# Performance work log

Hardware: AMD Instinct MI355X
Metric: run time of the kernel (lower is better)

## Reference

```python
import jax, jax.numpy as jnp
import numpy as np

B, S, HID = 2, 4096, 2048
NH, NKV, HD = 32, 8, 64
GROUPS = NH // NKV
ROPE_THETA = 10000.0


def _rope_cos_sin(seq_len, dim, dtype):
    inv_freq = 1.0 / (ROPE_THETA ** (jnp.arange(0, dim, 2, dtype=jnp.float32) / dim))
    pos = jnp.arange(seq_len, dtype=jnp.float32)
    freqs = pos[:, None] * inv_freq[None, :]          # [S, D/2]
    emb = jnp.concatenate([freqs, freqs], axis=-1)    # [S, D]
    return jnp.cos(emb).astype(dtype), jnp.sin(emb).astype(dtype)


def _rotate_half(x):
    x1, x2 = jnp.split(x, 2, axis=-1)
    return jnp.concatenate([-x2, x1], axis=-1)


def _apply_rope(x, cos, sin):
    # x: [B, H, S, D]; cos/sin: [S, D]
    return x * cos[None, None] + _rotate_half(x) * sin[None, None]


def kappa(x):
    return jax.nn.elu(x) + 1.0


def setup_inputs() -> dict:
    key = jax.random.key(0)
    ks = jax.random.split(key, 6)
    sc = 0.02
    return {
        "hidden_states": jax.random.normal(ks[0], (B, S, HID), jnp.float32),
        "Wq": jax.random.normal(ks[1], (HID, NH * HD), jnp.float32) * sc,
        "Wk": jax.random.normal(ks[2], (HID, NKV * HD), jnp.float32) * sc,
        "Wv": jax.random.normal(ks[3], (HID, NKV * HD), jnp.float32) * sc,
        "Wphi": jax.random.normal(ks[4], (HID, HID), jnp.float32) * sc,
        "Wo": jax.random.normal(ks[5], (HID, HID), jnp.float32) * sc,
    }


def reference(hidden_states, Wq, Wk, Wv, Wphi, Wo):
    bsz, q_len, _ = hidden_states.shape

    q = (hidden_states @ Wq).reshape(bsz, q_len, NH, HD).transpose(0, 2, 1, 3)   # [B,NH,S,D]
    k = (hidden_states @ Wk).reshape(bsz, q_len, NKV, HD).transpose(0, 2, 1, 3)  # [B,NKV,S,D]
    v = (hidden_states @ Wv).reshape(bsz, q_len, NKV, HD).transpose(0, 2, 1, 3)

    cos, sin = _rope_cos_sin(q_len, HD, hidden_states.dtype)
    q = _apply_rope(q, cos, sin)
    k = _apply_rope(k, cos, sin)

    # repeat_kv for GQA: [B,NKV,S,D] -> [B,NH,S,D]
    k = jnp.repeat(k, GROUPS, axis=1)
    v = jnp.repeat(v, GROUPS, axis=1)

    Qk = kappa(q)   # [B,NH,S,D]
    Kk = kappa(k)

    Qg = Qk.mean(axis=2)                                # [B,NH,D] global query
    logits = jnp.einsum("bnd,bnsd->bns", Qg, Kk)        # [B,NH,S]
    alpha = jax.nn.softmax(logits, axis=-1) * float(q_len)

    # KV aggregation: [B,NH,D,D] state
    outer_sum = jnp.einsum("bns,bnsd,bnsf->bndf", alpha, Kk, v)
    result_attn = jnp.einsum("bnsd,bndf->bnsf", Qk, outer_sum)  # [B,NH,S,D]

    X_phi = (hidden_states @ Wphi).reshape(bsz, q_len, NH, HD).transpose(0, 2, 1, 3)
    ctx = (X_phi * result_attn).transpose(0, 2, 1, 3).reshape(bsz, q_len, HID)
    return ctx @ Wo
```

## Files before the change

### kernel.cpp

```cpp
#include <hip/hip_runtime.h>
#include <hip/hip_bf16.h>

#define B_ 2
#define S_ 4096
#define HID_ 2048
#define NH_ 32
#define NKV_ 8
#define HD_ 64
#define GROUPS_ 4
#define NCH_ 32

typedef short short8 __attribute__((ext_vector_type(8)));
typedef float floatx4 __attribute__((ext_vector_type(4)));

__device__ __forceinline__ float bf2f(unsigned short u){
  union { unsigned int i; float f; } v; v.i = ((unsigned int)u) << 16; return v.f;
}
__device__ __forceinline__ unsigned short f2bf(float f){
  union { float f; unsigned int i; } v; v.f = f;
  unsigned int i = v.i;
  unsigned int r = (i + 0x7fffu + ((i >> 16) & 1u)) >> 16;
  return (unsigned short)r;
}

__device__ __forceinline__ void async_copy16(unsigned short* lds, const unsigned short* g){
  __builtin_amdgcn_global_load_lds((const __attribute__((address_space(1))) void*)g,
                                   (__attribute__((address_space(3))) void*)lds,
                                   16, 0, 0);
}

__global__ void conv_bf16(const float* __restrict__ x, unsigned short* __restrict__ y, int n4){
  int i = blockIdx.x * 256 + threadIdx.x;
  if (i < n4){
    float4 v = ((const float4*)x)[i];
    ushort4 o;
    o.x = f2bf(v.x); o.y = f2bf(v.y); o.z = f2bf(v.z); o.w = f2bf(v.w);
    ((ushort4*)y)[i] = o;
  }
}

__global__ void transpose_to_bf16(const float* __restrict__ W, unsigned short* __restrict__ Wt,
                                  int K, int N){
  __shared__ float tile[32][33];
  int n0 = blockIdx.x * 32, k0 = blockIdx.y * 32;
  int tx = threadIdx.x, ty = threadIdx.y;
  #pragma unroll
  for (int j = 0; j < 4; j++)
    tile[ty + j*8][tx] = W[(size_t)(k0 + ty + j*8) * N + n0 + tx];
  __syncthreads();
  #pragma unroll
  for (int j = 0; j < 4; j++)
    Wt[(size_t)(n0 + ty + j*8) * K + k0 + tx] = f2bf(tile[tx][ty + j*8]);
}

#define GTILE 16384

__global__ __launch_bounds__(512, 2) void gemm256(
    const unsigned short* __restrict__ A, const unsigned short* __restrict__ Bt,
    void* __restrict__ Cv, int M, int N, int K, int cbf16)
{
  __shared__ __align__(16) unsigned short As[2 * GTILE];
  __shared__ __align__(16) unsigned short Bs[2 * GTILE];

  const int tid = threadIdx.x;
  const int w = tid >> 6, lane = tid & 63;
  const int wr = w >> 2, wc = w & 3;
  const int l15 = lane & 15, quad = lane >> 4;

  const int nbx = N >> 8;
  int flat = blockIdx.y * nbx + blockIdx.x;
  int nwg  = nbx * (M >> 8);
  int cpx  = nwg >> 3;
  int swz  = (flat & 7) * cpx + (flat >> 3);
  int bx = swz % nbx, by = swz / nbx;
  const int m0 = by << 8, n0 = bx << 8;

  const int srow = (w << 3) + (lane >> 3);
  const int scc  = (lane & 7) ^ (lane >> 3);
  const unsigned short* gA = A  + (size_t)(m0 + srow) * K + scc * 8;
  const unsigned short* gB = Bt + (size_t)(n0 + srow) * K + scc * 8;
  const size_t rs64  = (size_t)64  * K;
  const size_t rs128 = (size_t)128 * K;
  unsigned short* lA0 = As + (w << 9);
  unsigned short* lB0 = Bs + (w << 9);

#define STAGE_A(bsel, h, t) do { \
    unsigned short* _d = lA0 + (bsel) * GTILE + (h) * 8192; \
    const unsigned short* _g = gA + (size_t)(h) * rs128 + (size_t)(t) * 64; \
    async_copy16(_d, _g); \
    async_copy16(_d + 4096, _g + rs64); \
  } while (0)
#define STAGE_B(bsel, h, t) do { \
    unsigned short* _d = lB0 + (bsel) * GTILE + (h) * 8192; \
    const unsigned short* _g = gB + (size_t)(h) * rs128 + (size_t)(t) * 64; \
    async_copy16(_d, _g); \
    async_copy16(_d + 4096, _g + rs64); \
  } while (0)
#define SCHED0 __builtin_amdgcn_sched_barrier(0)

  const int ks0  = ((quad     ^ (lane & 7)) << 3);
  const int ks1  = (((4+quad) ^ (lane & 7)) << 3);
  const int arow = (wr * 128 + l15) * 64;
  const int brow = (wc * 64  + l15) * 64;

  floatx4 acc[8][4] = {};
  short8 af[8][2], bfr[4][2];

  const int nt = K >> 6;

  STAGE_A(0, 0, 0); STAGE_A(0, 1, 0); STAGE_B(0, 0, 0); STAGE_B(0, 1, 0);
  if (nt > 1){
    STAGE_A(1, 0, 1); STAGE_A(1, 1, 1); STAGE_B(1, 0, 1); STAGE_B(1, 1, 1);
    asm volatile("s_waitcnt vmcnt(8)" ::: "memory");
  } else {
    asm volatile("s_waitcnt vmcnt(0)" ::: "memory");
  }
  SCHED0;
  __builtin_amdgcn_s_barrier();
  SCHED0;

  for (int T = 0; T < nt; ++T){
    const int cb = T & 1;
    const unsigned short* Ab = As + cb * GTILE;
    const unsigned short* Bb = Bs + cb * GTILE;

    #pragma unroll
    for (int m = 0; m < 4; ++m){
      af[m][0] = *(const short8*)(Ab + arow + m * 1024 + ks0);
      af[m][1] = *(const short8*)(Ab + arow + m * 1024 + ks1);
    }
    #pragma unroll
    for (int n = 0; n < 2; ++n){
      bfr[n][0] = *(const short8*)(Bb + brow + n * 1024 + ks0);
      bfr[n][1] = *(const short8*)(Bb + brow + n * 1024 + ks1);
    }
    SCHED0; __builtin_amdgcn_s_barrier(); SCHED0;
    __builtin_amdgcn_s_setprio(1);
    #pragma unroll
    for (int m = 0; m < 4; ++m)
      #pragma unroll
      for (int n = 0; n < 2; ++n){
        acc[m][n] = __builtin_amdgcn_mfma_f32_16x16x32_bf16(af[m][0], bfr[n][0], acc[m][n], 0, 0, 0);
        acc[m][n] = __builtin_amdgcn_mfma_f32_16x16x32_bf16(af[m][1], bfr[n][1], acc[m][n], 0, 0, 0);
      }
    __builtin_amdgcn_s_setprio(0);
    SCHED0; __builtin_amdgcn_s_barrier(); SCHED0;

    #pragma unroll
    for (int m = 0; m < 4; ++m){
      af[4+m][0] = *(const short8*)(Ab + arow + (4+m) * 1024 + ks0);
      af[4+m][1] = *(const short8*)(Ab + arow + (4+m) * 1024 + ks1);
    }
    #pragma unroll
    for (int n = 0; n < 2; ++n){
      bfr[2+n][0] = *(const short8*)(Bb + brow + (2+n) * 1024 + ks0);
      bfr[2+n][1] = *(const short8*)(Bb + brow + (2+n) * 1024 + ks1);
    }
    SCHED0; __builtin_amdgcn_s_barrier(); SCHED0;
    __builtin_amdgcn_s_setprio(1);
    #pragma unroll
    for (int m = 0; m < 4; ++m)
      #pragma unroll
      for (int n = 0; n < 2; ++n){
        acc[m][2+n] = __builtin_amdgcn_mfma_f32_16x16x32_bf16(af[m][0], bfr[2+n][0], acc[m][2+n], 0, 0, 0);
        acc[m][2+n] = __builtin_amdgcn_mfma_f32_16x16x32_bf16(af[m][1], bfr[2+n][1], acc[m][2+n], 0, 0, 0);
      }
    __builtin_amdgcn_s_setprio(0);
    SCHED0; __builtin_amdgcn_s_barrier(); SCHED0;

    if (T + 2 < nt){ STAGE_A(cb, 0, T + 2); STAGE_A(cb, 1, T + 2); }
    SCHED0; __builtin_amdgcn_s_barrier(); SCHED0;
    __builtin_amdgcn_s_setprio(1);
    #pragma unroll
    for (int m = 0; m < 4; ++m)
      #pragma unroll
      for (int n = 0; n < 2; ++n){
        acc[4+m][n] = __builtin_amdgcn_mfma_f32_16x16x32_bf16(af[4+m][0], bfr[n][0], acc[4+m][n], 0, 0, 0);
        acc[4+m][n] = __builtin_amdgcn_mfma_f32_16x16x32_bf16(af[4+m][1], bfr[n][1], acc[4+m][n], 0, 0, 0);
      }
    __builtin_amdgcn_s_setprio(0);
    SCHED0; __builtin_amdgcn_s_barrier(); SCHED0;

    if (T + 2 < nt){
      STAGE_B(cb, 0, T + 2); STAGE_B(cb, 1, T + 2);
      asm volatile("s_waitcnt vmcnt(8)" ::: "memory");
    } else {
      asm volatile("s_waitcnt vmcnt(0)" ::: "memory");
    }
    SCHED0; __builtin_amdgcn_s_barrier(); SCHED0;
    __builtin_amdgcn_s_setprio(1);
    #pragma unroll
    for (int m = 0; m < 4; ++m)
      #pragma unroll
      for (int n = 0; n < 2; ++n){
        acc[4+m][2+n] = __builtin_amdgcn_mfma_f32_16x16x32_bf16(af[4+m][0], bfr[2+n][0], acc[4+m][2+n], 0, 0, 0);
        acc[4+m][2+n] = __builtin_amdgcn_mfma_f32_16x16x32_bf16(af[4+m][1], bfr[2+n][1], acc[4+m][2+n], 0, 0, 0);
      }
    __builtin_amdgcn_s_setprio(0);
    SCHED0; __builtin_amdgcn_s_barrier(); SCHED0;
  }

#undef STAGE_A
#undef STAGE_B
#undef SCHED0

  if (cbf16){
    unsigned short* Cb = (unsigned short*)Cv;
    #pragma unroll
    for (int mi = 0; mi < 8; ++mi){
      const int row = m0 + wr * 128 + mi * 16 + quad * 4;
      #pragma unroll
      for (int ni = 0; ni < 4; ++ni){
        const int col = n0 + wc * 64 + ni * 16 + l15;
        #pragma unroll
        for (int r = 0; r < 4; ++r)
          Cb[(size_t)(row + r) * N + col] = f2bf(acc[mi][ni][r]);
      }
    }
  } else {
    float* Cf = (float*)Cv;
    #pragma unroll
    for (int mi = 0; mi < 8; ++mi){
      const int row = m0 + wr * 128 + mi * 16 + quad * 4;
      #pragma unroll
      for (int ni = 0; ni < 4; ++ni){
        const int col = n0 + wc * 64 + ni * 16 + l15;
        #pragma unroll
        for (int r = 0; r < 4; ++r)
          Cf[(size_t)(row + r) * N + col] = acc[mi][ni][r];
      }
    }
  }
}

__global__ void rope_kappa_q(const unsigned short* __restrict__ Qlin, unsigned short* __restrict__ Qk){
  int idx = blockIdx.x * 256 + threadIdx.x;
  int i = idx & 31;
  int n = (idx >> 5) & (NH_ - 1);
  int s = (idx >> 10) & (S_ - 1);
  int b = idx >> 22;
  float invf = exp2f(-(float)i * (13.287712379549449f / 32.0f));
  float ang = (float)s * invf;
  float c = cosf(ang), sn = sinf(ang);
  size_t in_o = ((size_t)(b * S_ + s) * NH_ + n) * HD_;
  float x1 = bf2f(Qlin[in_o + i]);
  float x2 = bf2f(Qlin[in_o + i + 32]);
  float r1 = x1 * c - x2 * sn;
  float r2 = x2 * c + x1 * sn;
  r1 = r1 > 0.f ? r1 + 1.f : __expf(r1);
  r2 = r2 > 0.f ? r2 + 1.f : __expf(r2);
  size_t o = ((size_t)(b * NH_ + n) * S_ + s) * HD_;
  Qk[o + i] = f2bf(r1);
  Qk[o + i + 32] = f2bf(r2);
}

__global__ void rope_kappa_k(const unsigned short* __restrict__ KVlin, unsigned short* __restrict__ Kk){
  int idx = blockIdx.x * 256 + threadIdx.x;
  int i = idx & 31;
  int kv = (idx >> 5) & (NKV_ - 1);
  int s = (idx >> 8) & (S_ - 1);
  int b = idx >> 20;
  float invf = exp2f(-(float)i * (13.287712379549449f / 32.0f));
  float ang = (float)s * invf;
  float c = cosf(ang), sn = sinf(ang);
  size_t in_o = (size_t)(b * S_ + s) * 1024 + kv * HD_;
  float x1 = bf2f(KVlin[in_o + i]);
  float x2 = bf2f(KVlin[in_o + i + 32]);
  float r1 = x1 * c - x2 * sn;
  float r2 = x2 * c + x1 * sn;
  r1 = r1 > 0.f ? r1 + 1.f : __expf(r1);
  r2 = r2 > 0.f ? r2 + 1.f : __expf(r2);
  size_t o = ((size_t)(b * NKV_ + kv) * S_ + s) * HD_;
  Kk[o + i] = f2bf(r1);
  Kk[o + i + 32] = f2bf(r2);
}

__global__ __launch_bounds__(256) void qg_mean(const unsigned short* __restrict__ Qk,
                                               float* __restrict__ Qg){
  int bn = blockIdx.x, chunk = blockIdx.y;
  int tid = threadIdx.x;
  int dgrp = tid & 7, sgrp = tid >> 3;
  const unsigned short* base = Qk + (size_t)bn * S_ * HD_
                             + (size_t)(chunk * 256 + sgrp) * HD_ + dgrp * 8;
  float acc[8] = {};
  #pragma unroll
  for (int i = 0; i < 8; i++){
    short8 v = *(const short8*)(base + (size_t)i * 32 * HD_);
    #pragma unroll
    for (int e = 0; e < 8; e++) acc[e] += bf2f((unsigned short)v[e]);
  }
  __shared__ float red[256][8];
  #pragma unroll
  for (int e = 0; e < 8; e++) red[tid][e] = acc[e];
  __syncthreads();
  if (tid < 64){
    int dg = tid >> 3, e = tid & 7;
    float s = 0.f;
    #pragma unroll
    for (int g = 0; g < 32; g++) s += red[g * 8 + dg][e];
    atomicAdd(&Qg[bn * 64 + tid], s * (1.0f / (float)S_));
  }
}

__global__ __launch_bounds__(256) void logits_kernel(const unsigned short* __restrict__ Kk,
                                                     const float* __restrict__ Qg,
                                                     float* __restrict__ logits){
  int bn = blockIdx.x, chunk = blockIdx.y;
  int b = bn / NH_, n = bn % NH_, kv = n / GROUPS_;
  int tid = threadIdx.x;
  __shared__ float qg[64];
  if (tid < 64) qg[tid] = Qg[bn * 64 + tid];
  __syncthreads();
  int s = chunk * 256 + tid;
  const unsigned short* row = Kk + ((size_t)(b * NKV_ + kv) * S_ + s) * HD_;
  float acc = 0.f;
  #pragma unroll
  for (int c = 0; c < 8; c++){
    short8 v = *(const short8*)(row + c * 8);
    #pragma unroll
    for (int e = 0; e < 8; e++) acc += qg[c * 8 + e] * bf2f((unsigned short)v[e]);
  }
  logits[(size_t)bn * S_ + s] = acc;
}

__global__ __launch_bounds__(256) void softmax_kernel(const float* __restrict__ logits,
                                                      float* __restrict__ alpha){
  int bn = blockIdx.x;
  int tid = threadIdx.x;
  float l[16];
  float mymax = -1e30f;
  #pragma unroll
  for (int j = 0; j < 16; j++){
    l[j] = logits[(size_t)bn * S_ + j * 256 + tid];
    mymax = fmaxf(mymax, l[j]);
  }
  __shared__ float red[256];
  red[tid] = mymax; __syncthreads();
  for (int st = 128; st > 0; st >>= 1){
    if (tid < st) red[tid] = fmaxf(red[tid], red[tid + st]);
    __syncthreads();
  }
  float gmax = red[0];
  __syncthreads();
  float mysum = 0.f;
  #pragma unroll
  for (int j = 0; j < 16; j++){ l[j] = __expf(l[j] - gmax); mysum += l[j]; }
  red[tid] = mysum; __syncthreads();
  for (int st = 128; st > 0; st >>= 1){
    if (tid < st) red[tid] += red[tid + st];
    __syncthreads();
  }
  float inv = (float)S_ / red[0];
  #pragma unroll
  for (int j = 0; j < 16; j++)
    alpha[(size_t)bn * S_ + j * 256 + tid] = l[j] * inv;
}

__global__ __launch_bounds__(256) void outer_sum_kernel(const unsigned short* __restrict__ Kk,
                                                        const unsigned short* __restrict__ KVlin,
                                                        const float* __restrict__ alpha,
                                                        float* __restrict__ part){
  int bkv = blockIdx.x, chunk = blockIdx.y;
  int b = bkv >> 3, kv = bkv & 7;
  int tid = threadIdx.x;
  int d = tid >> 2, fb = (tid & 3) * 16;
  __shared__ float ks[64][64];
  __shared__ float vs[64][64];
  __shared__ float as[4][64];
  float acc[4][16] = {};
  const unsigned short* kb = Kk + (size_t)(b * NKV_ + kv) * S_ * HD_;
  const int SPC = S_ / NCH_;

  for (int t = 0; t < SPC / 64; t++){
    int ss = chunk * SPC + t * 64;
    #pragma unroll
    for (int jj = 0; jj < 4; jj++){
      int idx4 = jj * 256 + tid;
      int si = idx4 >> 4, c4 = (idx4 & 15) * 4;
      ushort4 kv4 = *(const ushort4*)(kb + (size_t)(ss + si) * HD_ + c4);
      ks[si][c4]   = bf2f(kv4.x); ks[si][c4+1] = bf2f(kv4.y);
      ks[si][c4+2] = bf2f(kv4.z); ks[si][c4+3] = bf2f(kv4.w);
      ushort4 vv4 = *(const ushort4*)(KVlin + (size_t)(b * S_ + ss + si) * 1024 + 512 + kv * HD_ + c4);
      vs[si][c4]   = bf2f(vv4.x); vs[si][c4+1] = bf2f(vv4.y);
      vs[si][c4+2] = bf2f(vv4.z); vs[si][c4+3] = bf2f(vv4.w);
    }
    {
      int h = tid >> 6, si = tid & 63;
      as[h][si] = alpha[(size_t)(b * NH_ + kv * GROUPS_ + h) * S_ + ss + si];
    }
    __syncthreads();
    #pragma unroll 4
    for (int si = 0; si < 64; si++){
      float k = ks[si][d];
      float4 v0 = *(const float4*)&vs[si][fb];
      float4 v1 = *(const float4*)&vs[si][fb + 4];
      float4 v2 = *(const float4*)&vs[si][fb + 8];
      float4 v3 = *(const float4*)&vs[si][fb + 12];
      #pragma unroll
      for (int h = 0; h < 4; h++){
        float ak = as[h][si] * k;
        acc[h][0]  += ak * v0.x; acc[h][1]  += ak * v0.y; acc[h][2]  += ak * v0.z; acc[h][3]  += ak * v0.w;
        acc[h][4]  += ak * v1.x; acc[h][5]  += ak * v1.y; acc[h][6]  += ak * v1.z; acc[h][7]  += ak * v1.w;
        acc[h][8]  += ak * v2.x; acc[h][9]  += ak * v2.y; acc[h][10] += ak * v2.z; acc[h][11] += ak * v2.w;
        acc[h][12] += ak * v3.x; acc[h][13] += ak * v3.y; acc[h][14] += ak * v3.z; acc[h][15] += ak * v3.w;
      }
    }
    __syncthreads();
  }

  #pragma unroll
  for (int h = 0; h < 4; h++){
    float* pb = part + ((size_t)(chunk * 16 + bkv) * 4 + h) * 4096 + d * 64 + fb;
    #pragma unroll
    for (int j = 0; j < 4; j++)
      *(float4*)&pb[j * 4] = *(float4*)&acc[h][j * 4];
  }
}

__global__ __launch_bounds__(256) void osum_reduce_t(const float* __restrict__ part,
                                                     unsigned short* __restrict__ osumb){
  int bn = blockIdx.x;
  int tid = threadIdx.x;
  __shared__ float os[64][65];
  const float4* p4 = (const float4*)part;
  #pragma unroll
  for (int r = 0; r < 4; r++){
    int idx4 = r * 256 + tid;
    float4 s = {0.f, 0.f, 0.f, 0.f};
    #pragma unroll 8
    for (int c = 0; c < NCH_; c++){
      float4 v = p4[(size_t)c * 65536 + bn * 1024 + idx4];
      s.x += v.x; s.y += v.y; s.z += v.z; s.w += v.w;
    }
    int d = idx4 >> 4;
    int f0 = (idx4 & 15) * 4;
    os[d][f0] = s.x; os[d][f0+1] = s.y; os[d][f0+2] = s.z; os[d][f0+3] = s.w;
  }
  __syncthreads();
  int f = tid >> 2, d0 = (tid & 3) * 16;
  unsigned short hi[16], lo[16];
  #pragma unroll
  for (int j = 0; j < 16; j++){
    float x = os[d0 + j][f];
    unsigned short h = f2bf(x);
    hi[j] = h;
    lo[j] = f2bf(x - bf2f(h));
  }
  unsigned short* oh = osumb + ((size_t)bn * 2) * 4096 + (size_t)f * 64 + d0;
  unsigned short* ol = oh + 4096;
  *(short8*)(oh)     = *(const short8*)(hi);
  *(short8*)(oh + 8) = *(const short8*)(hi + 8);
  *(short8*)(ol)     = *(const short8*)(lo);
  *(short8*)(ol + 8) = *(const short8*)(lo + 8);
}

__global__ __launch_bounds__(256) void ctx_mfma(const unsigned short* __restrict__ Qk,
                                                const unsigned short* __restrict__ osumb,
                                                const unsigned short* __restrict__ Xphi,
                                                unsigned short* __restrict__ ctx){
  int bn = blockIdx.x, sc = blockIdx.y;
  int b = bn >> 5, n = bn & 31;
  int tid = threadIdx.x;
  int w = tid >> 6, lane = tid & 63;
  int l15 = lane & 15, quad = lane >> 4;

  const unsigned short* obase = osumb + ((size_t)bn * 2) * 4096;
  short8 bh[4][2], bl[4][2];
  #pragma unroll
  for (int nf = 0; nf < 4; nf++){
    int f = nf * 16 + l15;
    #pragma unroll
    for (int kh = 0; kh < 2; kh++){
      bh[nf][kh] = *(const short8*)(obase + (size_t)f * 64 + kh * 32 + quad * 8);
      bl[nf][kh] = *(const short8*)(obase + 4096 + (size_t)f * 64 + kh * 32 + quad * 8);
    }
  }

  int s0 = sc * 256 + w * 64;
  const unsigned short* qbase = Qk + ((size_t)bn * S_ + s0) * HD_;
  floatx4 acc[4][4] = {};
  #pragma unroll
  for (int m = 0; m < 4; m++){
    short8 a0 = *(const short8*)(qbase + (size_t)(m * 16 + l15) * HD_ + quad * 8);
    short8 a1 = *(const short8*)(qbase + (size_t)(m * 16 + l15) * HD_ + 32 + quad * 8);
    #pragma unroll
    for (int nf = 0; nf < 4; nf++){
      acc[m][nf] = __builtin_amdgcn_mfma_f32_16x16x32_bf16(a0, bh[nf][0], acc[m][nf], 0, 0, 0);
      acc[m][nf] = __builtin_amdgcn_mfma_f32_16x16x32_bf16(a1, bh[nf][1], acc[m][nf], 0, 0, 0);
      acc[m][nf] = __builtin_amdgcn_mfma_f32_16x16x32_bf16(a0, bl[nf][0], acc[m][nf], 0, 0, 0);
      acc[m][nf] = __builtin_amdgcn_mfma_f32_16x16x32_bf16(a1, bl[nf][1], acc[m][nf], 0, 0, 0);
    }
  }

  #pragma unroll
  for (int m = 0; m < 4; m++){
    #pragma unroll
    for (int r = 0; r < 4; r++){
      int s = s0 + m * 16 + quad * 4 + r;
      const unsigned short* xp = Xphi + ((size_t)(b * S_ + s) * NH_ + n) * HD_;
      unsigned short* cp = ctx + (size_t)(b * S_ + s) * HID_ + n * HD_;
      #pragma unroll
      for (int nf = 0; nf < 4; nf++){
        int f = nf * 16 + l15;
        cp[f] = f2bf(bf2f(xp[f]) * acc[m][nf][r]);
      }
    }
  }
}

extern "C" void kernel_launch(void* const* d_in, const int* in_sizes, int n_in,
                              void* d_out, int out_size, void* d_ws, size_t ws_size,
                              hipStream_t stream) {
  const float* hs   = (const float*)d_in[0];
  const float* Wq   = (const float*)d_in[1];
  const float* Wk   = (const float*)d_in[2];
  const float* Wv   = (const float*)d_in[3];
  const float* Wphi = (const float*)d_in[4];
  const float* Wo   = (const float*)d_in[5];
  float* out = (float*)d_out;

  char* ws = (char*)d_ws;
  const size_t M = (size_t)B_ * S_;
  size_t off = 0;
  auto alloc = [&](size_t bytes){ size_t o = off; off += (bytes + 255) & ~(size_t)255; return o; };

  size_t off_hsb   = alloc(M * HID_ * 2);
  size_t off_wqt   = alloc((size_t)HID_ * HID_ * 2);
  size_t off_wkvt  = alloc((size_t)HID_ * 1024 * 2);
  size_t off_wpt   = alloc((size_t)HID_ * HID_ * 2);
  size_t off_wot   = alloc((size_t)HID_ * HID_ * 2);
  size_t off_qlin  = alloc(M * HID_ * 2);
  size_t off_kvlin = alloc(M * 1024 * 2);
  size_t off_qk    = alloc(M * HID_ * 2);
  size_t off_kk    = alloc(M * 512 * 2);
  size_t off_qg    = alloc(64 * 64 * 4);
  size_t off_alph  = alloc((size_t)B_ * NH_ * S_ * 4);
  size_t off_osumb = alloc((size_t)64 * 2 * 4096 * 2);
  size_t off_ctx   = alloc(M * HID_ * 2);
  size_t off_part  = off_qlin;
  (void)ws_size;

  unsigned short* hsb  = (unsigned short*)(ws + off_hsb);
  unsigned short* wqt  = (unsigned short*)(ws + off_wqt);
  unsigned short* wkvt = (unsigned short*)(ws + off_wkvt);
  unsigned short* wpt  = (unsigned short*)(ws + off_wpt);
  unsigned short* wot  = (unsigned short*)(ws + off_wot);
  unsigned short* qlinb  = (unsigned short*)(ws + off_qlin);
  unsigned short* kvlinb = (unsigned short*)(ws + off_kvlin);
  unsigned short* qk = (unsigned short*)(ws + off_qk);
  unsigned short* kk = (unsigned short*)(ws + off_kk);
  float* qg   = (float*)(ws + off_qg);
  float* alph = (float*)(ws + off_alph);
  unsigned short* osumb = (unsigned short*)(ws + off_osumb);
  float* part = (float*)(ws + off_part);
  unsigned short* ctx = (unsigned short*)(ws + off_ctx);

  conv_bf16<<<(int)(M * HID_ / 4 / 256), 256, 0, stream>>>(hs, hsb, (int)(M * HID_ / 4));
  transpose_to_bf16<<<dim3(HID_/32, HID_/32), dim3(32,8), 0, stream>>>(Wq, wqt, HID_, HID_);
  transpose_to_bf16<<<dim3(512/32,  HID_/32), dim3(32,8), 0, stream>>>(Wk, wkvt, HID_, 512);
  transpose_to_bf16<<<dim3(512/32,  HID_/32), dim3(32,8), 0, stream>>>(Wv, wkvt + (size_t)512 * HID_, HID_, 512);
  transpose_to_bf16<<<dim3(HID_/32, HID_/32), dim3(32,8), 0, stream>>>(Wphi, wpt, HID_, HID_);
  transpose_to_bf16<<<dim3(HID_/32, HID_/32), dim3(32,8), 0, stream>>>(Wo, wot, HID_, HID_);
  gemm256<<<dim3(HID_/256, M/256), 512, 0, stream>>>(hsb, wqt, qlinb, (int)M, HID_, HID_, 1);
  gemm256<<<dim3(1024/256, M/256), 512, 0, stream>>>(hsb, wkvt, kvlinb, (int)M, 1024, HID_, 1);
  rope_kappa_q<<<(int)(M * NH_ * 32 / 256), 256, 0, stream>>>(qlinb, qk);
  rope_kappa_k<<<(int)(M * NKV_ * 32 / 256), 256, 0, stream>>>(kvlinb, kk);
  hipMemsetAsync(qg, 0, 64 * 64 * 4, stream);
  qg_mean<<<dim3(B_ * NH_, S_ / 256), 256, 0, stream>>>(qk, qg);
  logits_kernel<<<dim3(B_ * NH_, S_ / 256), 256, 0, stream>>>(kk, qg, alph);
  softmax_kernel<<<B_ * NH_, 256, 0, stream>>>(alph, alph);
  outer_sum_kernel<<<dim3(B_ * NKV_, NCH_), 256, 0, stream>>>(kk, kvlinb, alph, part);
  osum_reduce_t<<<64, 256, 0, stream>>>(part, osumb);
  gemm256<<<dim3(HID_/256, M/256), 512, 0, stream>>>(hsb, wpt, qlinb, (int)M, HID_, HID_, 1);
  ctx_mfma<<<dim3(B_ * NH_, S_ / 64 / 4), 256, 0, stream>>>(qk, osumb, qlinb, ctx);
  gemm256<<<dim3(HID_/256, M/256), 512, 0, stream>>>(ctx, wot, out, (int)M, HID_, HID_, 0);
}
```

Before: 552.7 us.

## Fuse Q, KV and Phi projections into one concatenated-weight GEMM

The transposed Wq, Wk, Wv and Wphi are packed into one [5120 x 2048] bf16 weight, so a single GEMM launch produces all projection outputs into one row-major buffer with stride 5120. The RoPE/kappa, outer-sum and context kernels now read at offsets into this buffer. Workspace is shrunk by aliasing the bf16 input, the partial sums and ctx onto one region, relying on their lifetimes not overlapping. The MFMA inner loops are also reordered to put the k-step outermost, so consecutive MFMAs target different accumulators instead of chaining back-to-back on the same one. The aim is fewer launches and better tail-wave use across one larger grid, at the cost of strided output rows and a tighter buffer-reuse dependency order.

```diff
diff --git a/kernel.cpp b/kernel.cpp
--- a/kernel.cpp
+++ b/kernel.cpp
@@ -9,6 +9,7 @@
 #define HD_ 64
 #define GROUPS_ 4
 #define NCH_ 32
+#define NLIN_ 5120
 
 typedef short short8 __attribute__((ext_vector_type(8)));
 typedef float floatx4 __attribute__((ext_vector_type(4)));
@@ -137,12 +138,12 @@
     SCHED0; __builtin_amdgcn_s_barrier(); SCHED0;
     __builtin_amdgcn_s_setprio(1);
     #pragma unroll
-    for (int m = 0; m < 4; ++m)
-      #pragma unroll
-      for (int n = 0; n < 2; ++n){
-        acc[m][n] = __builtin_amdgcn_mfma_f32_16x16x32_bf16(af[m][0], bfr[n][0], acc[m][n], 0, 0, 0);
-        acc[m][n] = __builtin_amdgcn_mfma_f32_16x16x32_bf16(af[m][1], bfr[n][1], acc[m][n], 0, 0, 0);
-      }
+    for (int k = 0; k < 2; ++k)
+      #pragma unroll
+      for (int m = 0; m < 4; ++m)
+        #pragma unroll
+        for (int n = 0; n < 2; ++n)
+          acc[m][n] = __builtin_amdgcn_mfma_f32_16x16x32_bf16(af[m][k], bfr[n][k], acc[m][n], 0, 0, 0);
     __builtin_amdgcn_s_setprio(0);
     SCHED0; __builtin_amdgcn_s_barrier(); SCHED0;
 
@@ -159,12 +160,12 @@
     SCHED0; __builtin_amdgcn_s_barrier(); SCHED0;
     __builtin_amdgcn_s_setprio(1);
     #pragma unroll
-    for (int m = 0; m < 4; ++m)
-      #pragma unroll
-      for (int n = 0; n < 2; ++n){
-        acc[m][2+n] = __builtin_amdgcn_mfma_f32_16x16x32_bf16(af[m][0], bfr[2+n][0], acc[m][2+n], 0, 0, 0);
-        acc[m][2+n] = __builtin_amdgcn_mfma_f32_16x16x32_bf16(af[m][1], bfr[2+n][1], acc[m][2+n], 0, 0, 0);
-      }
+    for (int k = 0; k < 2; ++k)
+      #pragma unroll
+      for (int m = 0; m < 4; ++m)
+        #pragma unroll
+        for (int n = 0; n < 2; ++n)
+          acc[m][2+n] = __builtin_amdgcn_mfma_f32_16x16x32_bf16(af[m][k], bfr[2+n][k], acc[m][2+n], 0, 0, 0);
     __builtin_amdgcn_s_setprio(0);
     SCHED0; __builtin_amdgcn_s_barrier(); SCHED0;
 
@@ -172,12 +173,12 @@
     SCHED0; __builtin_amdgcn_s_barrier(); SCHED0;
     __builtin_amdgcn_s_setprio(1);
     #pragma unroll
-    for (int m = 0; m < 4; ++m)
-      #pragma unroll
-      for (int n = 0; n < 2; ++n){
-        acc[4+m][n] = __builtin_amdgcn_mfma_f32_16x16x32_bf16(af[4+m][0], bfr[n][0], acc[4+m][n], 0, 0, 0);
-        acc[4+m][n] = __builtin_amdgcn_mfma_f32_16x16x32_bf16(af[4+m][1], bfr[n][1], acc[4+m][n], 0, 0, 0);
-      }
+    for (int k = 0; k < 2; ++k)
+      #pragma unroll
+      for (int m = 0; m < 4; ++m)
+        #pragma unroll
+        for (int n = 0; n < 2; ++n)
+          acc[4+m][n] = __builtin_amdgcn_mfma_f32_16x16x32_bf16(af[4+m][k], bfr[n][k], acc[4+m][n], 0, 0, 0);
     __builtin_amdgcn_s_setprio(0);
     SCHED0; __builtin_amdgcn_s_barrier(); SCHED0;
 
@@ -190,12 +191,12 @@
     SCHED0; __builtin_amdgcn_s_barrier(); SCHED0;
     __builtin_amdgcn_s_setprio(1);
     #pragma unroll
-    for (int m = 0; m < 4; ++m)
-      #pragma unroll
-      for (int n = 0; n < 2; ++n){
-        acc[4+m][2+n] = __builtin_amdgcn_mfma_f32_16x16x32_bf16(af[4+m][0], bfr[2+n][0], acc[4+m][2+n], 0, 0, 0);
-        acc[4+m][2+n] = __builtin_amdgcn_mfma_f32_16x16x32_bf16(af[4+m][1], bfr[2+n][1], acc[4+m][2+n], 0, 0, 0);
-      }
+    for (int k = 0; k < 2; ++k)
+      #pragma unroll
+      for (int m = 0; m < 4; ++m)
+        #pragma unroll
+        for (int n = 0; n < 2; ++n)
+          acc[4+m][2+n] = __builtin_amdgcn_mfma_f32_16x16x32_bf16(af[4+m][k], bfr[2+n][k], acc[4+m][2+n], 0, 0, 0);
     __builtin_amdgcn_s_setprio(0);
     SCHED0; __builtin_amdgcn_s_barrier(); SCHED0;
   }
@@ -233,7 +234,7 @@
   }
 }
 
-__global__ void rope_kappa_q(const unsigned short* __restrict__ Qlin, unsigned short* __restrict__ Qk){
+__global__ void rope_kappa_q(const unsigned short* __restrict__ lin, unsigned short* __restrict__ Qk){
   int idx = blockIdx.x * 256 + threadIdx.x;
   int i = idx & 31;
   int n = (idx >> 5) & (NH_ - 1);
@@ -242,9 +243,9 @@
   float invf = exp2f(-(float)i * (13.287712379549449f / 32.0f));
   float ang = (float)s * invf;
   float c = cosf(ang), sn = sinf(ang);
-  size_t in_o = ((size_t)(b * S_ + s) * NH_ + n) * HD_;
-  float x1 = bf2f(Qlin[in_o + i]);
-  float x2 = bf2f(Qlin[in_o + i + 32]);
+  size_t in_o = (size_t)(b * S_ + s) * NLIN_ + n * HD_;
+  float x1 = bf2f(lin[in_o + i]);
+  float x2 = bf2f(lin[in_o + i + 32]);
   float r1 = x1 * c - x2 * sn;
   float r2 = x2 * c + x1 * sn;
   r1 = r1 > 0.f ? r1 + 1.f : __expf(r1);
@@ -254,7 +255,7 @@
   Qk[o + i + 32] = f2bf(r2);
 }
 
-__global__ void rope_kappa_k(const unsigned short* __restrict__ KVlin, unsigned short* __restrict__ Kk){
+__global__ void rope_kappa_k(const unsigned short* __restrict__ lin, unsigned short* __restrict__ Kk){
   int idx = blockIdx.x * 256 + threadIdx.x;
   int i = idx & 31;
   int kv = (idx >> 5) & (NKV_ - 1);
@@ -263,9 +264,9 @@
   float invf = exp2f(-(float)i * (13.287712379549449f / 32.0f));
   float ang = (float)s * invf;
   float c = cosf(ang), sn = sinf(ang);
-  size_t in_o = (size_t)(b * S_ + s) * 1024 + kv * HD_;
-  float x1 = bf2f(KVlin[in_o + i]);
-  float x2 = bf2f(KVlin[in_o + i + 32]);
+  size_t in_o = (size_t)(b * S_ + s) * NLIN_ + 2048 + kv * HD_;
+  float x1 = bf2f(lin[in_o + i]);
+  float x2 = bf2f(lin[in_o + i + 32]);
   float r1 = x1 * c - x2 * sn;
   float r2 = x2 * c + x1 * sn;
   r1 = r1 > 0.f ? r1 + 1.f : __expf(r1);
@@ -357,7 +358,7 @@
 }
 
 __global__ __launch_bounds__(256) void outer_sum_kernel(const unsigned short* __restrict__ Kk,
-                                                        const unsigned short* __restrict__ KVlin,
+                                                        const unsigned short* __restrict__ lin,
                                                         const float* __restrict__ alpha,
                                                         float* __restrict__ part){
   int bkv = blockIdx.x, chunk = blockIdx.y;
@@ -380,7 +381,7 @@
       ushort4 kv4 = *(const ushort4*)(kb + (size_t)(ss + si) * HD_ + c4);
       ks[si][c4]   = bf2f(kv4.x); ks[si][c4+1] = bf2f(kv4.y);
       ks[si][c4+2] = bf2f(kv4.z); ks[si][c4+3] = bf2f(kv4.w);
-      ushort4 vv4 = *(const ushort4*)(KVlin + (size_t)(b * S_ + ss + si) * 1024 + 512 + kv * HD_ + c4);
+      ushort4 vv4 = *(const ushort4*)(lin + (size_t)(b * S_ + ss + si) * NLIN_ + 2560 + kv * HD_ + c4);
       vs[si][c4]   = bf2f(vv4.x); vs[si][c4+1] = bf2f(vv4.y);
       vs[si][c4+2] = bf2f(vv4.z); vs[si][c4+3] = bf2f(vv4.w);
     }
@@ -456,7 +457,7 @@
 
 __global__ __launch_bounds__(256) void ctx_mfma(const unsigned short* __restrict__ Qk,
                                                 const unsigned short* __restrict__ osumb,
-                                                const unsigned short* __restrict__ Xphi,
+                                                const unsigned short* __restrict__ lin,
                                                 unsigned short* __restrict__ ctx){
   int bn = blockIdx.x, sc = blockIdx.y;
   int b = bn >> 5, n = bn & 31;
@@ -497,7 +498,7 @@
     #pragma unroll
     for (int r = 0; r < 4; r++){
       int s = s0 + m * 16 + quad * 4 + r;
-      const unsigned short* xp = Xphi + ((size_t)(b * S_ + s) * NH_ + n) * HD_;
+      const unsigned short* xp = lin + (size_t)(b * S_ + s) * NLIN_ + 3072 + n * HD_;
       unsigned short* cp = ctx + (size_t)(b * S_ + s) * HID_ + n * HD_;
       #pragma unroll
       for (int nf = 0; nf < 4; nf++){
@@ -524,54 +525,44 @@
   size_t off = 0;
   auto alloc = [&](size_t bytes){ size_t o = off; off += (bytes + 255) & ~(size_t)255; return o; };
 
-  size_t off_hsb   = alloc(M * HID_ * 2);
-  size_t off_wqt   = alloc((size_t)HID_ * HID_ * 2);
-  size_t off_wkvt  = alloc((size_t)HID_ * 1024 * 2);
-  size_t off_wpt   = alloc((size_t)HID_ * HID_ * 2);
+  size_t off_x     = alloc(M * HID_ * 4);
+  size_t off_wcat  = alloc((size_t)NLIN_ * HID_ * 2);
   size_t off_wot   = alloc((size_t)HID_ * HID_ * 2);
-  size_t off_qlin  = alloc(M * HID_ * 2);
-  size_t off_kvlin = alloc(M * 1024 * 2);
+  size_t off_lin   = alloc(M * NLIN_ * 2);
   size_t off_qk    = alloc(M * HID_ * 2);
   size_t off_kk    = alloc(M * 512 * 2);
   size_t off_qg    = alloc(64 * 64 * 4);
   size_t off_alph  = alloc((size_t)B_ * NH_ * S_ * 4);
   size_t off_osumb = alloc((size_t)64 * 2 * 4096 * 2);
-  size_t off_ctx   = alloc(M * HID_ * 2);
-  size_t off_part  = off_qlin;
   (void)ws_size;
 
-  unsigned short* hsb  = (unsigned short*)(ws + off_hsb);
-  unsigned short* wqt  = (unsigned short*)(ws + off_wqt);
-  unsigned short* wkvt = (unsigned short*)(ws + off_wkvt);
-  unsigned short* wpt  = (unsigned short*)(ws + off_wpt);
+  unsigned short* hsb  = (unsigned short*)(ws + off_x);
+  float*          part = (float*)(ws + off_x);
+  unsigned short* ctx  = (unsigned short*)(ws + off_x);
+  unsigned short* wcat = (unsigned short*)(ws + off_wcat);
   unsigned short* wot  = (unsigned short*)(ws + off_wot);
-  unsigned short* qlinb  = (unsigned short*)(ws + off_qlin);
-  unsigned short* kvlinb = (unsigned short*)(ws + off_kvlin);
+  unsigned short* lin  = (unsigned short*)(ws + off_lin);
   unsigned short* qk = (unsigned short*)(ws + off_qk);
   unsigned short* kk = (unsigned short*)(ws + off_kk);
   float* qg   = (float*)(ws + off_qg);
   float* alph = (float*)(ws + off_alph);
   unsigned short* osumb = (unsigned short*)(ws + off_osumb);
-  float* part = (float*)(ws + off_part);
-  unsigned short* ctx = (unsigned short*)(ws + off_ctx);
 
   conv_bf16<<<(int)(M * HID_ / 4 / 256), 256, 0, stream>>>(hs, hsb, (int)(M * HID_ / 4));
-  transpose_to_bf16<<<dim3(HID_/32, HID_/32), dim3(32,8), 0, stream>>>(Wq, wqt, HID_, HID_);
-  transpose_to_bf16<<<dim3(512/32,  HID_/32), dim3(32,8), 0, stream>>>(Wk, wkvt, HID_, 512);
-  transpose_to_bf16<<<dim3(512/32,  HID_/32), dim3(32,8), 0, stream>>>(Wv, wkvt + (size_t)512 * HID_, HID_, 512);
-  transpose_to_bf16<<<dim3(HID_/32, HID_/32), dim3(32,8), 0, stream>>>(Wphi, wpt, HID_, HID_);
-  transpose_to_bf16<<<dim3(HID_/32, HID_/32), dim3(32,8), 0, stream>>>(Wo, wot, HID_, HID_);
-  gemm256<<<dim3(HID_/256, M/256), 512, 0, stream>>>(hsb, wqt, qlinb, (int)M, HID_, HID_, 1);
-  gemm256<<<dim3(1024/256, M/256), 512, 0, stream>>>(hsb, wkvt, kvlinb, (int)M, 1024, HID_, 1);
-  rope_kappa_q<<<(int)(M * NH_ * 32 / 256), 256, 0, stream>>>(qlinb, qk);
-  rope_kappa_k<<<(int)(M * NKV_ * 32 / 256), 256, 0, stream>>>(kvlinb, kk);
+  transpose_to_bf16<<<dim3(HID_/32, HID_/32), dim3(32,8), 0, stream>>>(Wq,   wcat,                          HID_, HID_);
+  transpose_to_bf16<<<dim3(512/32,  HID_/32), dim3(32,8), 0, stream>>>(Wk,   wcat + (size_t)2048 * HID_,    HID_, 512);
+  transpose_to_bf16<<<dim3(512/32,  HID_/32), dim3(32,8), 0, stream>>>(Wv,   wcat + (size_t)2560 * HID_,    HID_, 512);
+  transpose_to_bf16<<<dim3(HID_/32, HID_/32), dim3(32,8), 0, stream>>>(Wphi, wcat + (size_t)3072 * HID_,    HID_, HID_);
+  transpose_to_bf16<<<dim3(HID_/32, HID_/32), dim3(32,8), 0, stream>>>(Wo,   wot,                           HID_, HID_);
+  gemm256<<<dim3(NLIN_/256, M/256), 512, 0, stream>>>(hsb, wcat, lin, (int)M, NLIN_, HID_, 1);
+  rope_kappa_q<<<(int)(M * NH_ * 32 / 256), 256, 0, stream>>>(lin, qk);
+  rope_kappa_k<<<(int)(M * NKV_ * 32 / 256), 256, 0, stream>>>(lin, kk);
   hipMemsetAsync(qg, 0, 64 * 64 * 4, stream);
   qg_mean<<<dim3(B_ * NH_, S_ / 256), 256, 0, stream>>>(qk, qg);
   logits_kernel<<<dim3(B_ * NH_, S_ / 256), 256, 0, stream>>>(kk, qg, alph);
   softmax_kernel<<<B_ * NH_, 256, 0, stream>>>(alph, alph);
-  outer_sum_kernel<<<dim3(B_ * NKV_, NCH_), 256, 0, stream>>>(kk, kvlinb, alph, part);
+  outer_sum_kernel<<<dim3(B_ * NKV_, NCH_), 256, 0, stream>>>(kk, lin, alph, part);
   osum_reduce_t<<<64, 256, 0, stream>>>(part, osumb);
-  gemm256<<<dim3(HID_/256, M/256), 512, 0, stream>>>(hsb, wpt, qlinb, (int)M, HID_, HID_, 1);
-  ctx_mfma<<<dim3(B_ * NH_, S_ / 64 / 4), 256, 0, stream>>>(qk, osumb, qlinb, ctx);
+  ctx_mfma<<<dim3(B_ * NH_, S_ / 64 / 4), 256, 0, stream>>>(qk, osumb, lin, ctx);
   gemm256<<<dim3(HID_/256, M/256), 512, 0, stream>>>(ctx, wot, out, (int)M, HID_, HID_, 0);
 }
```

New measurement: 545.0 us. Within noise of the previous version (-1.4%).
